# Kernel optimization log

Hardware: AMD Instinct MI355X
Metric: run time of the kernel (lower is better)

Reference implementation:

```python
import jax, jax.numpy as jnp
import numpy as np

DIM = 1024
SRC_DIM = 1152
NUM_HEADS = 16
HEAD_DIM = DIM // NUM_HEADS  # 64
ROPE_BASE = 10000.0


def rope_tables(seq_len, head_dim):
    # matches RotaryPositionEmbedding: inv_freq over even indices, emb = cat([freqs, freqs])
    inv_freq = 1.0 / (ROPE_BASE ** (jnp.arange(0, head_dim, 2, dtype=jnp.float32) / head_dim))
    t = jnp.arange(seq_len, dtype=jnp.float32)
    freqs = t[:, None] * inv_freq[None, :]          # (L, D/2)
    emb = jnp.concatenate([freqs, freqs], axis=-1)  # (L, D)
    return jnp.cos(emb), jnp.sin(emb)


def rotate_half(x):
    # interleaved rotation as in the torch code
    x1 = x[..., ::2]
    x2 = x[..., 1::2]
    return jnp.stack((-x2, x1), axis=-1).reshape(x.shape)


def apply_rope(t, cos, sin):
    # t: (B, H, L, D); cos/sin: (L, D)
    return t * cos[None, None] + rotate_half(t) * sin[None, None]


def setup_inputs() -> dict:
    key = jax.random.key(0)
    ks = jax.random.split(key, 10)
    B, T, K = 2, 2048, 2048
    s_q = 1.0 / np.sqrt(DIM)
    s_kv = 1.0 / np.sqrt(SRC_DIM)
    return {
        "x": jax.random.normal(ks[0], (B, T, DIM), jnp.float32),
        "context": jax.random.normal(ks[1], (B, K, SRC_DIM), jnp.float32),
        "Wq": jax.random.normal(ks[2], (DIM, DIM), jnp.float32) * s_q,
        "bq": jnp.zeros((DIM,), jnp.float32),
        "Wk": jax.random.normal(ks[3], (DIM, SRC_DIM), jnp.float32) * s_kv,
        "bk": jnp.zeros((DIM,), jnp.float32),
        "Wv": jax.random.normal(ks[4], (DIM, SRC_DIM), jnp.float32) * s_kv,
        "bv": jnp.zeros((DIM,), jnp.float32),
        "Wo": jax.random.normal(ks[5], (DIM, DIM), jnp.float32) * s_q,
        "bo": jnp.zeros((DIM,), jnp.float32),
    }


def reference(x, context, Wq, bq, Wk, bk, Wv, bv, Wo, bo):
    B, T, C = x.shape
    K = context.shape[1]
    H, D = NUM_HEADS, HEAD_DIM

    q = x @ Wq.T + bq                 # (B, T, C)
    k = context @ Wk.T + bk           # (B, K, C)
    v = context @ Wv.T + bv           # (B, K, C)

    q = q.reshape(B, T, H, D).transpose(0, 2, 1, 3)  # (B, H, T, D)
    k = k.reshape(B, K, H, D).transpose(0, 2, 1, 3)  # (B, H, K, D)
    v = v.reshape(B, K, H, D).transpose(0, 2, 1, 3)

    cos_q, sin_q = rope_tables(T, D)
    cos_k, sin_k = rope_tables(K, D)
    q = apply_rope(q, cos_q, sin_q)
    k = apply_rope(k, cos_k, sin_k)

    scale = 1.0 / np.sqrt(D).astype(np.float32)
    scores = jnp.einsum('bhtd,bhkd->bhtk', q, k) * scale  # (B, H, T, K)
    weights = jax.nn.softmax(scores, axis=-1)
    out = jnp.einsum('bhtk,bhkd->bhtd', weights, v)        # (B, H, T, D)
    out = out.transpose(0, 2, 1, 3).reshape(B, T, C)
    return out @ Wo.T + bo
```

## Files before the change

kernel.cpp:

```cpp
#include <hip/hip_runtime.h>
#include <hip/hip_bf16.h>
#include <stdint.h>

typedef unsigned short u16;
typedef __attribute__((ext_vector_type(8))) short bf16x8;
typedef __attribute__((ext_vector_type(8))) unsigned short u16x8;
typedef __attribute__((ext_vector_type(4))) float f32x4;

#define BM 128
#define BN 128
#define BK 32
#define QSCALE 0.18033688f

__device__ __forceinline__ u16 f2bf(float f) {
    union { float f; uint32_t u; } v; v.f = f;
    uint32_t r = v.u + 0x7FFFu + ((v.u >> 16) & 1u);
    return (u16)(r >> 16);
}

__device__ __forceinline__ uint32_t cvt_pk_bf16(float lo, float hi) {
    uint32_t r;
    asm("v_cvt_pk_bf16_f32 %0, %1, %2" : "=v"(r) : "v"(lo), "v"(hi));
    return r;
}

__device__ __forceinline__ float fexp2(float x) {
    float r;
    asm volatile("v_exp_f32 %0, %1\n\ts_nop 0" : "=v"(r) : "v"(x));
    return r;
}

__device__ __forceinline__ void gload_lds16(const void* g, void* l) {
    __builtin_amdgcn_global_load_lds(
        (const __attribute__((address_space(1))) void*)(g),
        (__attribute__((address_space(3))) void*)(l),
        16, 0, 0);
}

__global__ void prep_kernel(const float* __restrict__ x, const float* __restrict__ ctx,
                            const float* __restrict__ Wq, const float* __restrict__ Wk,
                            const float* __restrict__ Wv, const float* __restrict__ Wo,
                            u16* __restrict__ xb, u16* __restrict__ cb,
                            u16* __restrict__ wqb, u16* __restrict__ wkb,
                            u16* __restrict__ wvb, u16* __restrict__ wob,
                            float2* __restrict__ cs) {
    int t = blockIdx.x * 256 + threadIdx.x;
    if (t < 3342336) {
        const float* src; u16* dst; int base;
        if      (t < 1048576) { src = x;   dst = xb;  base = 0; }
        else if (t < 2228224) { src = ctx; dst = cb;  base = 1048576; }
        else if (t < 2490368) { src = Wq;  dst = wqb; base = 2228224; }
        else if (t < 2785280) { src = Wk;  dst = wkb; base = 2490368; }
        else if (t < 3080192) { src = Wv;  dst = wvb; base = 2785280; }
        else                  { src = Wo;  dst = wob; base = 3080192; }
        int i = (t - base) * 4;
        float4 v = *reinterpret_cast<const float4*>(src + i);
        ushort4 o = { f2bf(v.x), f2bf(v.y), f2bf(v.z), f2bf(v.w) };
        *reinterpret_cast<ushort4*>(dst + i) = o;
    } else {
        int idx = t - 3342336;
        int tt = idx >> 5, j = idx & 31;
        float invf = 1.0f / powf(10000.0f, (float)(2 * j) / 64.0f);
        float ang = (float)tt * invf;
        cs[idx] = make_float2(cosf(ang), sinf(ang));
    }
}

__global__ __launch_bounds__(256, 4)
void qkv_gemm(const u16* __restrict__ xb, const u16* __restrict__ cb,
              const u16* __restrict__ wqb, const u16* __restrict__ wkb,
              const u16* __restrict__ wvb,
              const float* __restrict__ bq, const float* __restrict__ bk,
              const float* __restrict__ bv,
              u16* __restrict__ qo, u16* __restrict__ ko, u16* __restrict__ vo,
              const float2* __restrict__ cs)
{
    __shared__ __align__(16) u16 As[BM * BK];
    __shared__ __align__(16) u16 Bs[BN * BK];
    const int bid = blockIdx.x;
    const int wg = (bid & 7) * 96 + (bid >> 3);
    const int seg = wg >> 8, inner = wg & 255;
    const u16* A; const u16* Bm; const float* bias; u16* C;
    int N, K, mbase, nbase, rope, brow;
    float oscale;
    if (seg == 0)      { A = xb;  Bm = wqb; bias = bq; C = qo; N = 1024; K = 1024; rope = 1; brow = 0; oscale = QSCALE; nbase = (inner & 7) * BN;  mbase = (inner >> 3) * BM; }
    else if (seg == 1) { A = cb;  Bm = wkb; bias = bk; C = ko; N = 1024; K = 1152; rope = 1; brow = 0; oscale = 1.0f;   nbase = (inner & 7) * BN;  mbase = (inner >> 3) * BM; }
    else               { A = wvb; Bm = cb;  bias = bv; C = vo; N = 4096; K = 1152; rope = 0; brow = 1; oscale = 1.0f;   nbase = (inner & 31) * BN; mbase = (inner >> 5) * BM; }

    const int tid = threadIdx.x;
    const int wid = tid >> 6, lane = tid & 63;
    const int wr = wid >> 1, wc = wid & 1;
    const int l15 = lane & 15, l4 = lane >> 4;
    const int srow = lane >> 2;
    const int scol = (lane & 3) * 8;

    f32x4 acc[4][4];
#pragma unroll
    for (int i = 0; i < 4; i++)
#pragma unroll
        for (int j = 0; j < 4; j++) acc[i][j] = (f32x4){0.f, 0.f, 0.f, 0.f};

    for (int k0 = 0; k0 < K; k0 += BK) {
#pragma unroll
        for (int q = 0; q < 2; ++q) {
            int segr = wid * 2 + q;
            int row = segr * 16 + srow;
            gload_lds16(A  + (size_t)(mbase + row) * K + k0 + scol, (void*)(As + segr * 512));
            gload_lds16(Bm + (size_t)(nbase + row) * K + k0 + scol, (void*)(Bs + segr * 512));
        }
        __syncthreads();
        bf16x8 af[4], bfv[4];
#pragma unroll
        for (int i = 0; i < 4; i++)
            af[i] = *(const bf16x8*)(As + (wr * 64 + i * 16 + l15) * BK + l4 * 8);
#pragma unroll
        for (int j = 0; j < 4; j++)
            bfv[j] = *(const bf16x8*)(Bs + (wc * 64 + j * 16 + l15) * BK + l4 * 8);
#pragma unroll
        for (int i = 0; i < 4; i++)
#pragma unroll
            for (int j = 0; j < 4; j++)
                acc[i][j] = __builtin_amdgcn_mfma_f32_16x16x32_bf16(af[i], bfv[j], acc[i][j], 0, 0, 0);
        __syncthreads();
    }

#pragma unroll
    for (int i = 0; i < 4; i++) {
#pragma unroll
        for (int j = 0; j < 4; j++) {
#pragma unroll
            for (int r = 0; r < 4; r++) {
                int row = mbase + wr * 64 + i * 16 + l4 * 4 + r;
                int col = nbase + wc * 64 + j * 16 + l15;
                float v = acc[i][j][r] + (brow ? bias[row] : bias[col]);
                if (rope) {
                    float part = __shfl_xor(v, 1);
                    float2 c2 = cs[(row & 2047) * 32 + (col & 31)];
                    v = v * c2.x + ((col & 1) ? part * c2.y : -part * c2.y);
                    v *= oscale;
                }
                C[(size_t)row * N + col] = f2bf(v);
            }
        }
    }
}

__global__ __launch_bounds__(256, 2)
void gemm_out(const u16* __restrict__ A, const u16* __restrict__ B,
              const float* __restrict__ bias, float* __restrict__ C,
              int M, int N, int K)
{
    __shared__ __align__(16) u16 As[2][BM * BK];
    __shared__ __align__(16) u16 Bs[2][64 * BK];
    const int tid = threadIdx.x;
    const int wid = tid >> 6, lane = tid & 63;
    const int wr = wid >> 1, wc = wid & 1;
    const int l15 = lane & 15, l4 = lane >> 4;
    const int mbase = blockIdx.y * BM, nbase = blockIdx.x * 64;
    const int srow = lane >> 2;
    const int scol = (lane & 3) * 8;
    const int nk = K >> 5;

    f32x4 acc[4][2];
#pragma unroll
    for (int i = 0; i < 4; i++)
#pragma unroll
        for (int j = 0; j < 2; j++) acc[i][j] = (f32x4){0.f, 0.f, 0.f, 0.f};

    auto stage = [&](int bs, int k0) {
#pragma unroll
        for (int q = 0; q < 2; ++q) {
            int seg = wid * 2 + q;
            int row = seg * 16 + srow;
            gload_lds16(A + (size_t)(mbase + row) * K + k0 + scol, (void*)(&As[bs][seg * 512]));
        }
        {
            int row = wid * 16 + srow;
            gload_lds16(B + (size_t)(nbase + row) * K + k0 + scol, (void*)(&Bs[bs][wid * 512]));
        }
    };

    stage(0, 0);
    __syncthreads();
    int buf = 0;
    for (int ks = 0; ks < nk; ++ks) {
        if (ks + 1 < nk) stage(buf ^ 1, (ks + 1) * BK);
        bf16x8 af[4], bfv[2];
#pragma unroll
        for (int i = 0; i < 4; i++)
            af[i] = *(const bf16x8*)(&As[buf][(wr * 64 + i * 16 + l15) * BK + l4 * 8]);
#pragma unroll
        for (int j = 0; j < 2; j++)
            bfv[j] = *(const bf16x8*)(&Bs[buf][(wc * 32 + j * 16 + l15) * BK + l4 * 8]);
#pragma unroll
        for (int i = 0; i < 4; i++)
#pragma unroll
            for (int j = 0; j < 2; j++)
                acc[i][j] = __builtin_amdgcn_mfma_f32_16x16x32_bf16(af[i], bfv[j], acc[i][j], 0, 0, 0);
        __syncthreads();
        buf ^= 1;
    }

#pragma unroll
    for (int i = 0; i < 4; i++)
#pragma unroll
        for (int j = 0; j < 2; j++)
#pragma unroll
            for (int r = 0; r < 4; r++) {
                int row = mbase + wr * 64 + i * 16 + l4 * 4 + r;
                int col = nbase + wc * 32 + j * 16 + l15;
                C[(size_t)row * N + col] = acc[i][j][r] + bias[col];
            }
}

__device__ __forceinline__ int invrow(int R) {
    return 32 * (R >> 5) + 8 * ((R >> 2) & 3) + 4 * ((R >> 4) & 1) + (R & 3);
}

__global__ __launch_bounds__(256, 4)
void attn_kernel(const u16* __restrict__ Qb, const u16* __restrict__ Kb,
                 const u16* __restrict__ VT, u16* __restrict__ Ob)
{
    const int qt = blockIdx.x;
    const int bh = blockIdx.y;
    const int b = bh >> 4, h = bh & 15;
    __shared__ __align__(16) u16 Ks[2][4096];
    __shared__ __align__(16) u16 Vs[2][4096];
    const int tid = threadIdx.x, wv = tid >> 6, lane = tid & 63;
    const int l15 = lane & 15, l4 = lane >> 4;

    const int r8 = lane >> 3;
    const int cp = lane & 7;
    const int cl = cp ^ r8;
    const int L0 = 2 * wv, L1 = 2 * wv + 1;
    const int RK0 = L0 * 8 + r8, RK1 = L1 * 8 + r8;
    const u16* ksrc0 = Kb + (size_t)(b * 2048 + invrow(RK0)) * 1024 + h * 64 + cl * 8;
    const u16* ksrc1 = Kb + (size_t)(b * 2048 + invrow(RK1)) * 1024 + h * 64 + cl * 8;
    const u16* vsrc0 = VT + (size_t)(h * 64 + RK0) * 4096 + b * 2048 + cl * 8;
    const u16* vsrc1 = VT + (size_t)(h * 64 + RK1) * 4096 + b * 2048 + cl * 8;

    const u16* qrow = Qb + (size_t)(b * 2048 + qt * 64 + wv * 16 + l15) * 1024 + h * 64;
    bf16x8 qf0 = *(const bf16x8*)(qrow + l4 * 8);
    bf16x8 qf1 = *(const bf16x8*)(qrow + 32 + l4 * 8);

    const int swz = l15 & 7;
    const int q0o = (l4 ^ swz) * 8;
    const int q1o = ((4 + l4) ^ swz) * 8;

    f32x4 accO[4];
    float denom = 0.f;
#pragma unroll
    for (int i = 0; i < 4; i++) accO[i] = (f32x4){0.f, 0.f, 0.f, 0.f};

    auto stage = [&](int bs, int kt) {
        gload_lds16(ksrc0 + (size_t)kt * 65536, (void*)&Ks[bs][L0 * 512]);
        gload_lds16(ksrc1 + (size_t)kt * 65536, (void*)&Ks[bs][L1 * 512]);
        gload_lds16(vsrc0 + kt * 64,            (void*)&Vs[bs][L0 * 512]);
        gload_lds16(vsrc1 + kt * 64,            (void*)&Vs[bs][L1 * 512]);
    };

    stage(0, 0);
    __syncthreads();

    int buf = 0;
    for (int kt = 0; kt < 32; ++kt) {
        if (kt < 31) stage(buf ^ 1, kt + 1);

        f32x4 s[4];
#pragma unroll
        for (int j = 0; j < 4; j++) s[j] = (f32x4){0.f, 0.f, 0.f, 0.f};
        __builtin_amdgcn_s_setprio(1);
#pragma unroll
        for (int j = 0; j < 4; j++) {
            const u16* rp = &Ks[buf][(j * 16 + l15) * 64];
            bf16x8 a0 = *(const bf16x8*)(rp + q0o);
            bf16x8 a1 = *(const bf16x8*)(rp + q1o);
            s[j] = __builtin_amdgcn_mfma_f32_16x16x32_bf16(a0, qf0, s[j], 0, 0, 0);
            s[j] = __builtin_amdgcn_mfma_f32_16x16x32_bf16(a1, qf1, s[j], 0, 0, 0);
        }
        __builtin_amdgcn_s_setprio(0);

        float p[4][4];
        float rs = 0.f;
#pragma unroll
        for (int j = 0; j < 4; j++)
#pragma unroll
            for (int r = 0; r < 4; r++) {
                p[j][r] = fexp2(s[j][r]);
                rs += p[j][r];
            }
        rs += __shfl_xor(rs, 16);
        rs += __shfl_xor(rs, 32);
        denom += rs;

        union { uint32_t u[4]; bf16x8 v; } B0u, B1u;
        B0u.u[0] = cvt_pk_bf16(p[0][0], p[0][1]);
        B0u.u[1] = cvt_pk_bf16(p[0][2], p[0][3]);
        B0u.u[2] = cvt_pk_bf16(p[1][0], p[1][1]);
        B0u.u[3] = cvt_pk_bf16(p[1][2], p[1][3]);
        B1u.u[0] = cvt_pk_bf16(p[2][0], p[2][1]);
        B1u.u[1] = cvt_pk_bf16(p[2][2], p[2][3]);
        B1u.u[2] = cvt_pk_bf16(p[3][0], p[3][1]);
        B1u.u[3] = cvt_pk_bf16(p[3][2], p[3][3]);

        __builtin_amdgcn_s_setprio(1);
#pragma unroll
        for (int i = 0; i < 4; i++) {
            const u16* vp = &Vs[buf][(i * 16 + l15) * 64];
            bf16x8 v0 = *(const bf16x8*)(vp + q0o);
            bf16x8 v1 = *(const bf16x8*)(vp + q1o);
            accO[i] = __builtin_amdgcn_mfma_f32_16x16x32_bf16(v0, B0u.v, accO[i], 0, 0, 0);
            accO[i] = __builtin_amdgcn_mfma_f32_16x16x32_bf16(v1, B1u.v, accO[i], 0, 0, 0);
        }
        __builtin_amdgcn_s_setprio(0);
        __syncthreads();
        buf ^= 1;
    }

    float rd = 1.0f / denom;
    u16* orow = Ob + (size_t)(b * 2048 + qt * 64 + wv * 16 + l15) * 1024 + h * 64;
#pragma unroll
    for (int i = 0; i < 4; i++) {
        uint2 st;
        st.x = cvt_pk_bf16(accO[i][0] * rd, accO[i][1] * rd);
        st.y = cvt_pk_bf16(accO[i][2] * rd, accO[i][3] * rd);
        *(uint2*)(orow + i * 16 + l4 * 4) = st;
    }
}

extern "C" void kernel_launch(void* const* d_in, const int* in_sizes, int n_in,
                              void* d_out, int out_size, void* d_ws, size_t ws_size,
                              hipStream_t stream) {
    const float* x   = (const float*)d_in[0];
    const float* ctx = (const float*)d_in[1];
    const float* Wq  = (const float*)d_in[2];
    const float* bq  = (const float*)d_in[3];
    const float* Wk  = (const float*)d_in[4];
    const float* bk  = (const float*)d_in[5];
    const float* Wv  = (const float*)d_in[6];
    const float* bv  = (const float*)d_in[7];
    const float* Wo  = (const float*)d_in[8];
    const float* bo  = (const float*)d_in[9];
    float* out = (float*)d_out;

    char* ws = (char*)d_ws;
    size_t off = 0;
    auto alloc = [&](size_t bytes) { void* p = ws + off; off += (bytes + 255) & ~255ULL; return p; };
    u16* x_bf  = (u16*)alloc(4096ULL * 1024 * 2);
    u16* c_bf  = (u16*)alloc(4096ULL * 1152 * 2);
    u16* wq_bf = (u16*)alloc(1024ULL * 1024 * 2);
    u16* wk_bf = (u16*)alloc(1024ULL * 1152 * 2);
    u16* wv_bf = (u16*)alloc(1024ULL * 1152 * 2);
    u16* wo_bf = (u16*)alloc(1024ULL * 1024 * 2);
    float2* cs = (float2*)alloc(2048ULL * 32 * 8);
    u16* q_bf  = (u16*)alloc(4096ULL * 1024 * 2);
    u16* k_bf  = (u16*)alloc(4096ULL * 1024 * 2);
    u16* vT    = (u16*)alloc(1024ULL * 4096 * 2);
    u16* a_bf  = (u16*)alloc(4096ULL * 1024 * 2);

    prep_kernel<<<13312, 256, 0, stream>>>(x, ctx, Wq, Wk, Wv, Wo,
                                           x_bf, c_bf, wq_bf, wk_bf, wv_bf, wo_bf, cs);
    qkv_gemm<<<768, 256, 0, stream>>>(x_bf, c_bf, wq_bf, wk_bf, wv_bf,
                                      bq, bk, bv, q_bf, k_bf, vT, cs);
    attn_kernel<<<dim3(32, 32), 256, 0, stream>>>(q_bf, k_bf, vT, a_bf);
    gemm_out<<<dim3(16, 32), 256, 0, stream>>>(a_bf, wo_bf, bo, out, 4096, 1024, 1024);
}
```

Baseline: 142.5 us.

## Double QKV GEMM K-tile to 64 with XOR-swizzled LDS layout

The QKV projection GEMM now stages a K-slab of 64 instead of 32 per iteration, which halves the number of barrier pairs per K. The LDS tile uses an XOR swizzle (column chunk ^ row&7) on both the global-to-LDS write and the fragment reads to avoid bank conflicts with the wider 128-byte rows. MFMA issue is wrapped in s_setprio. Shared memory doubles to 32KB per block and launch bounds drop occupancy from 4 to 3 blocks per CU, trading fewer resident waves for less sync overhead.

```diff
diff --git a/kernel.cpp b/kernel.cpp
--- a/kernel.cpp
+++ b/kernel.cpp
@@ -10,6 +10,7 @@
 #define BM 128
 #define BN 128
 #define BK 32
+#define QBK 64
 #define QSCALE 0.18033688f
 
 __device__ __forceinline__ u16 f2bf(float f) {
@@ -66,7 +67,7 @@
     }
 }
 
-__global__ __launch_bounds__(256, 4)
+__global__ __launch_bounds__(256, 3)
 void qkv_gemm(const u16* __restrict__ xb, const u16* __restrict__ cb,
               const u16* __restrict__ wqb, const u16* __restrict__ wkb,
               const u16* __restrict__ wvb,
@@ -75,8 +76,8 @@
               u16* __restrict__ qo, u16* __restrict__ ko, u16* __restrict__ vo,
               const float2* __restrict__ cs)
 {
-    __shared__ __align__(16) u16 As[BM * BK];
-    __shared__ __align__(16) u16 Bs[BN * BK];
+    __shared__ __align__(16) u16 As[BM * QBK];
+    __shared__ __align__(16) u16 Bs[BN * QBK];
     const int bid = blockIdx.x;
     const int wg = (bid & 7) * 96 + (bid >> 3);
     const int seg = wg >> 8, inner = wg & 255;
@@ -91,8 +92,9 @@
     const int wid = tid >> 6, lane = tid & 63;
     const int wr = wid >> 1, wc = wid & 1;
     const int l15 = lane & 15, l4 = lane >> 4;
-    const int srow = lane >> 2;
-    const int scol = (lane & 3) * 8;
+    const int r8 = lane >> 3;
+    const int cp = lane & 7;
+    const int cl = cp ^ r8;
 
     f32x4 acc[4][4];
 #pragma unroll
@@ -100,27 +102,38 @@
 #pragma unroll
         for (int j = 0; j < 4; j++) acc[i][j] = (f32x4){0.f, 0.f, 0.f, 0.f};
 
-    for (int k0 = 0; k0 < K; k0 += BK) {
-#pragma unroll
-        for (int q = 0; q < 2; ++q) {
-            int segr = wid * 2 + q;
-            int row = segr * 16 + srow;
-            gload_lds16(A  + (size_t)(mbase + row) * K + k0 + scol, (void*)(As + segr * 512));
-            gload_lds16(Bm + (size_t)(nbase + row) * K + k0 + scol, (void*)(Bs + segr * 512));
+    for (int k0 = 0; k0 < K; k0 += QBK) {
+#pragma unroll
+        for (int q = 0; q < 4; ++q) {
+            int sg = wid * 4 + q;
+            int row = sg * 8 + r8;
+            gload_lds16(A  + (size_t)(mbase + row) * K + k0 + cl * 8, (void*)(As + sg * 512));
+            gload_lds16(Bm + (size_t)(nbase + row) * K + k0 + cl * 8, (void*)(Bs + sg * 512));
         }
         __syncthreads();
-        bf16x8 af[4], bfv[4];
-#pragma unroll
-        for (int i = 0; i < 4; i++)
-            af[i] = *(const bf16x8*)(As + (wr * 64 + i * 16 + l15) * BK + l4 * 8);
-#pragma unroll
-        for (int j = 0; j < 4; j++)
-            bfv[j] = *(const bf16x8*)(Bs + (wc * 64 + j * 16 + l15) * BK + l4 * 8);
-#pragma unroll
-        for (int i = 0; i < 4; i++)
-#pragma unroll
-            for (int j = 0; j < 4; j++)
-                acc[i][j] = __builtin_amdgcn_mfma_f32_16x16x32_bf16(af[i], bfv[j], acc[i][j], 0, 0, 0);
+        bf16x8 af[2][4], bfv[2][4];
+#pragma unroll
+        for (int kk = 0; kk < 2; kk++) {
+#pragma unroll
+            for (int i = 0; i < 4; i++) {
+                int r = wr * 64 + i * 16 + l15;
+                af[kk][i] = *(const bf16x8*)(As + r * 64 + (((kk * 4 + l4) ^ (r & 7)) * 8));
+            }
+#pragma unroll
+            for (int j = 0; j < 4; j++) {
+                int r = wc * 64 + j * 16 + l15;
+                bfv[kk][j] = *(const bf16x8*)(Bs + r * 64 + (((kk * 4 + l4) ^ (r & 7)) * 8));
+            }
+        }
+        __builtin_amdgcn_s_setprio(1);
+#pragma unroll
+        for (int kk = 0; kk < 2; kk++)
+#pragma unroll
+            for (int i = 0; i < 4; i++)
+#pragma unroll
+                for (int j = 0; j < 4; j++)
+                    acc[i][j] = __builtin_amdgcn_mfma_f32_16x16x32_bf16(af[kk][i], bfv[kk][j], acc[i][j], 0, 0, 0);
+        __builtin_amdgcn_s_setprio(0);
         __syncthreads();
     }
 
```

Measured after the change: 139.9 us. Within noise of the previous version (-1.8%).
